# Kernel optimization log

Measured on AMD Instinct MI355X. Metric: run time of the kernel, lower is better.

The kernel has to match this reference:

```python
import jax, jax.numpy as jnp
import numpy as np

N_NODES = 100000
N_EDGES = 1600000
D_IN = 128
D_HID = 128
N_CLS = 16
N_GRAPHS = 64


def setup_inputs() -> dict:
    key = jax.random.key(0)
    ks = jax.random.split(key, 12)
    h = jax.random.normal(ks[0], (N_NODES, D_IN), dtype=jnp.float32)
    src = jax.random.randint(ks[1], (N_EDGES,), 0, N_NODES, dtype=jnp.int32)
    dst = jax.random.randint(ks[2], (N_EDGES,), 0, N_NODES, dtype=jnp.int32)
    graph_ids = jnp.sort(jax.random.randint(ks[3], (N_NODES,), 0, N_GRAPHS, dtype=jnp.int32))
    s = 1.0 / np.sqrt(D_IN)
    W1_self = jax.random.uniform(ks[4], (D_IN, D_HID), jnp.float32, -s, s)
    W1_neigh = jax.random.uniform(ks[5], (D_IN, D_HID), jnp.float32, -s, s)
    b1 = jnp.zeros((D_HID,), jnp.float32)
    s2 = 1.0 / np.sqrt(D_HID)
    W2_self = jax.random.uniform(ks[6], (D_HID, D_HID), jnp.float32, -s2, s2)
    W2_neigh = jax.random.uniform(ks[7], (D_HID, D_HID), jnp.float32, -s2, s2)
    b2 = jnp.zeros((D_HID,), jnp.float32)
    Wc = jax.random.uniform(ks[8], (D_HID, N_CLS), jnp.float32, -s2, s2)
    bc = jnp.zeros((N_CLS,), jnp.float32)
    return {"h": h, "src": src, "dst": dst, "graph_ids": graph_ids, "num_graphs": N_GRAPHS,
            "W1_self": W1_self, "W1_neigh": W1_neigh, "b1": b1,
            "W2_self": W2_self, "W2_neigh": W2_neigh, "b2": b2,
            "Wc": Wc, "bc": bc}


def _sage_conv(h, src, dst, W_self, W_neigh, b):
    # DGL SAGEConv 'mean': out = fc_self(h) + fc_neigh(mean of in-neighbor feats) + bias
    n = h.shape[0]
    msg = jnp.take(h, src, axis=0)                               # [E, d] gather
    agg = jax.ops.segment_sum(msg, dst, num_segments=n)          # [N, d] scatter-add
    deg = jax.ops.segment_sum(jnp.ones((src.shape[0],), h.dtype), dst, num_segments=n)
    neigh = agg / jnp.maximum(deg, 1.0)[:, None]                 # mean, zero-degree safe
    return h @ W_self + neigh @ W_neigh + b


def reference(h, src, dst, graph_ids, num_graphs,
              W1_self, W1_neigh, b1, W2_self, W2_neigh, b2, Wc, bc):
    x = jax.nn.relu(_sage_conv(h, src, dst, W1_self, W1_neigh, b1))
    x = _sage_conv(x, src, dst, W2_self, W2_neigh, b2)
    # dgl.mean_nodes: per-graph mean over node features
    gsum = jax.ops.segment_sum(x, graph_ids, num_segments=num_graphs)    # [G, d]
    gcnt = jax.ops.segment_sum(jnp.ones((x.shape[0],), x.dtype), graph_ids, num_segments=num_graphs)
    hg = gsum / jnp.maximum(gcnt, 1.0)[:, None]
    return hg @ Wc + bc                                                  # [G, num_classes]
```

## Files before the change

kernel.cpp:

```cpp
#include <hip/hip_runtime.h>

#define D        128
#define N_GRAPHS 64
#define N_CLS    16
#define LDA      40
#define SLOTS    48
#define CAP      8192
#define NCH      768

typedef unsigned int   uint;
typedef unsigned short ushort;
typedef __attribute__((ext_vector_type(8))) short short8;
typedef __attribute__((ext_vector_type(4))) float f32x4;

__device__ inline ushort f2b(float f) {
    uint u = __float_as_uint(f);
    u += 0x7fffu + ((u >> 16) & 1u);
    return (ushort)(u >> 16);
}


__global__ __launch_bounds__(256) void k_part(
    const int* __restrict__ src, const int* __restrict__ dst,
    int* __restrict__ bcount, uint* __restrict__ ebuf, int E, int NB) {
    __shared__ int hist[512], base[512], lcur[512];
    int t = threadIdx.x;
    int per = (E + gridDim.x - 1) / gridDim.x;
    int e0 = blockIdx.x * per;
    int e1 = min(e0 + per, E);
    for (int i = t; i < NB; i += 256) { hist[i] = 0; lcur[i] = 0; }
    __syncthreads();
    for (int e = e0 + t; e < e1; e += 256) atomicAdd(&hist[dst[e] >> 8], 1);
    __syncthreads();
    for (int i = t; i < NB; i += 256)
        base[i] = hist[i] ? atomicAdd(&bcount[i], hist[i]) : 0;
    __syncthreads();
    for (int e = e0 + t; e < e1; e += 256) {
        int dd = dst[e];
        int b = dd >> 8;
        int off = atomicAdd(&lcur[b], 1);
        int pos = base[b] + off;
        if (pos < CAP)
            ebuf[(size_t)b * CAP + pos] = ((uint)src[e] << 8) | (uint)(dd & 255);
    }
}


__global__ __launch_bounds__(256) void k_part2(
    const int* __restrict__ src, const int* __restrict__ dst,
    int* __restrict__ bcount2, uint* __restrict__ ebuf2, int E, int NB) {
    __shared__ int hist[512], base[512], lcur[512];
    int t = threadIdx.x;
    int per = (E + gridDim.x - 1) / gridDim.x;
    int e0 = blockIdx.x * per;
    int e1 = min(e0 + per, E);
    for (int i = t; i < NB; i += 256) { hist[i] = 0; lcur[i] = 0; }
    __syncthreads();
    for (int e = e0 + t; e < e1; e += 256) atomicAdd(&hist[src[e] >> 8], 1);
    __syncthreads();
    for (int i = t; i < NB; i += 256)
        base[i] = hist[i] ? atomicAdd(&bcount2[i], hist[i]) : 0;
    __syncthreads();
    for (int e = e0 + t; e < e1; e += 256) {
        int ss = src[e];
        int b = ss >> 8;
        int off = atomicAdd(&lcur[b], 1);
        int pos = base[b] + off;
        if (pos < CAP)
            ebuf2[(size_t)b * CAP + pos] = ((uint)dst[e] << 8) | (uint)(ss & 255);
    }
}


__global__ __launch_bounds__(1024) void k_bucket(
    const uint* __restrict__ ebuf, const int* __restrict__ bcount,
    int* __restrict__ csrf, int* __restrict__ deg, float* __restrict__ invdeg,
    int N) {
    __shared__ int ldeg[256];
    __shared__ int lcsr[256 * SLOTS];
    int b = blockIdx.x, t = threadIdx.x;
    if (t < 256) ldeg[t] = 0;
    __syncthreads();
    int cnt = bcount[b];
    if (cnt > CAP) cnt = CAP;
    const uint* __restrict__ eb = ebuf + (size_t)b * CAP;
    for (int i = t; i < cnt; i += 1024) {
        uint r = eb[i];
        int dl = r & 255;
        int sl = atomicAdd(&ldeg[dl], 1);
        if (sl < SLOTS) lcsr[dl * SLOTS + sl] = (int)(r >> 8);
    }
    __syncthreads();
    int n0 = b << 8;
    int lim = (N - n0) * SLOTS;
    if (lim > 256 * SLOTS) lim = 256 * SLOTS;
    for (int i = t; i < lim; i += 1024)
        csrf[(size_t)n0 * SLOTS + i] = lcsr[i];
    if (t < 256 && n0 + t < N) {
        int d = ldeg[t];
        deg[n0 + t] = d;
        invdeg[n0 + t] = 1.0f / (float)(d > 1 ? d : 1);
    }
}


__global__ __launch_bounds__(1024) void k_wbucket(
    const uint* __restrict__ ebuf2, const int* __restrict__ bcount2,
    const int* __restrict__ gid, const float* __restrict__ invdeg,
    float* __restrict__ wc, int N) {
    __shared__ float lwc[256 * 64];
    int b = blockIdx.x, t = threadIdx.x;
    for (int i = t; i < 256 * 64; i += 1024) lwc[i] = 0.f;
    __syncthreads();
    int cnt = bcount2[b];
    if (cnt > CAP) cnt = CAP;
    const uint* __restrict__ eb = ebuf2 + (size_t)b * CAP;
    for (int i = t; i < cnt; i += 1024) {
        uint r = eb[i];
        int d  = (int)(r >> 8);
        int sl = (int)(r & 255u);
        atomicAdd(&lwc[sl * 64 + gid[d]], invdeg[d]);
    }
    __syncthreads();
    int n0 = b << 8;
    int lim = (N - n0) < 256 ? (N - n0) * 64 : 256 * 64;
    for (int i = t; i < lim; i += 1024)
        wc[(size_t)n0 * 64 + i] = lwc[i];
}

__global__ void k_gbound(const int* __restrict__ gid, int* __restrict__ gstart, int N) {
    int g = threadIdx.x;
    if (g > N_GRAPHS) return;
    int lo = 0, hi = N;
    while (lo < hi) {
        int mid = (lo + hi) >> 1;
        if (gid[mid] < g) lo = mid + 1; else hi = mid;
    }
    gstart[g] = lo;
}


__global__ void k_cast(const float* __restrict__ x, ushort* __restrict__ y, int total4) {
    int i = blockIdx.x * 256 + threadIdx.x;
    if (i < total4) {
        float4 v = ((const float4*)x)[i];
        ushort4 o;
        o.x = f2b(v.x); o.y = f2b(v.y); o.z = f2b(v.z); o.w = f2b(v.w);
        ((ushort4*)y)[i] = o;
    }
}

__global__ void k_castw(const float* __restrict__ Ws, const float* __restrict__ Wn,
                        ushort* __restrict__ wT) {
    int i = blockIdx.x * 256 + threadIdx.x;
    int c = i >> 8, k = i & 255;
    float v = (k < 128) ? Ws[k * 128 + c] : Wn[(k - 128) * 128 + c];
    wT[c * 256 + k] = f2b(v);
}


__global__ __launch_bounds__(256) void k_aggb(
    const ushort* __restrict__ fb, const int* __restrict__ deg,
    const int* __restrict__ csrf, const float* __restrict__ invdeg,
    ushort* __restrict__ outb, int N) {
    int lane = threadIdx.x & 63;
    int n = blockIdx.x * 4 + (threadIdx.x >> 6);
    if (n >= N) return;
    int d = deg[n];
    if (d > SLOTS) d = SLOTS;
    const int* __restrict__ lst = csrf + (size_t)n * SLOTS;
    int ej = lane >> 4;
    int cg = lane & 15;

    float acc[8];
#pragma unroll
    for (int i = 0; i < 8; i++) acc[i] = 0.f;

    int e = ej;
    for (; e + 4 < d; e += 8) {
        int s0 = lst[e];
        int s1 = lst[e + 4];
        uint4 v0 = *(const uint4*)(fb + (size_t)s0 * D + cg * 8);
        uint4 v1 = *(const uint4*)(fb + (size_t)s1 * D + cg * 8);
        acc[0] += __uint_as_float(v0.x << 16);
        acc[1] += __uint_as_float(v0.x & 0xffff0000u);
        acc[2] += __uint_as_float(v0.y << 16);
        acc[3] += __uint_as_float(v0.y & 0xffff0000u);
        acc[4] += __uint_as_float(v0.z << 16);
        acc[5] += __uint_as_float(v0.z & 0xffff0000u);
        acc[6] += __uint_as_float(v0.w << 16);
        acc[7] += __uint_as_float(v0.w & 0xffff0000u);
        acc[0] += __uint_as_float(v1.x << 16);
        acc[1] += __uint_as_float(v1.x & 0xffff0000u);
        acc[2] += __uint_as_float(v1.y << 16);
        acc[3] += __uint_as_float(v1.y & 0xffff0000u);
        acc[4] += __uint_as_float(v1.z << 16);
        acc[5] += __uint_as_float(v1.z & 0xffff0000u);
        acc[6] += __uint_as_float(v1.w << 16);
        acc[7] += __uint_as_float(v1.w & 0xffff0000u);
    }
    for (; e < d; e += 4) {
        int s = lst[e];
        uint4 v = *(const uint4*)(fb + (size_t)s * D + cg * 8);
        acc[0] += __uint_as_float(v.x << 16);
        acc[1] += __uint_as_float(v.x & 0xffff0000u);
        acc[2] += __uint_as_float(v.y << 16);
        acc[3] += __uint_as_float(v.y & 0xffff0000u);
        acc[4] += __uint_as_float(v.z << 16);
        acc[5] += __uint_as_float(v.z & 0xffff0000u);
        acc[6] += __uint_as_float(v.w << 16);
        acc[7] += __uint_as_float(v.w & 0xffff0000u);
    }
#pragma unroll
    for (int i = 0; i < 8; i++) {
        acc[i] += __shfl_xor(acc[i], 16);
        acc[i] += __shfl_xor(acc[i], 32);
    }
    if (ej == 0) {
        float id = invdeg[n];
        uint4 o;
        o.x = (uint)f2b(acc[0] * id) | ((uint)f2b(acc[1] * id) << 16);
        o.y = (uint)f2b(acc[2] * id) | ((uint)f2b(acc[3] * id) << 16);
        o.z = (uint)f2b(acc[4] * id) | ((uint)f2b(acc[5] * id) << 16);
        o.w = (uint)f2b(acc[6] * id) | ((uint)f2b(acc[7] * id) << 16);
        *(uint4*)(outb + (size_t)n * D + cg * 8) = o;
    }
}


__global__ __launch_bounds__(256, 2) void k_mm1m(
    const ushort* __restrict__ hb, const ushort* __restrict__ nbb,
    const ushort* __restrict__ wT, const float* __restrict__ b,
    ushort* __restrict__ x1b, int N) {
    __shared__ __align__(16) ushort As[128 * LDA];
    __shared__ __align__(16) ushort Bs[128 * LDA];
    int t    = threadIdx.x;
    int w    = t >> 6;
    int lane = t & 63;
    int m    = lane & 15;
    int quad = lane >> 4;
    int n0   = blockIdx.x * 128;

    f32x4 acc[2][8];
#pragma unroll
    for (int rt = 0; rt < 2; rt++)
#pragma unroll
        for (int ct = 0; ct < 8; ct++) acc[rt][ct] = (f32x4){0.f, 0.f, 0.f, 0.f};

#pragma unroll 1
    for (int kc = 0; kc < 8; kc++) {
        int k0 = kc * 32;
        const ushort* __restrict__ A = (k0 < 128) ? hb : nbb;
        int ka = k0 & 127;
        __syncthreads();
#pragma unroll
        for (int i = 0; i < 2; i++) {
            int linear = i * 256 + t;
            int row = linear >> 2;
            int q   = linear & 3;
            int nn = n0 + row;
            uint4 v = make_uint4(0u, 0u, 0u, 0u);
            if (nn < N) v = *(const uint4*)(A + (size_t)nn * D + ka + q * 8);
            *(uint4*)(&As[row * LDA + q * 8]) = v;
        }
#pragma unroll
        for (int i = 0; i < 2; i++) {
            int linear = i * 256 + t;
            int col = linear >> 2;
            int q   = linear & 3;
            uint4 v = *(const uint4*)(wT + (size_t)col * 256 + k0 + q * 8);
            *(uint4*)(&Bs[col * LDA + q * 8]) = v;
        }
        __syncthreads();
        short8 af[2], bf[8];
#pragma unroll
        for (int rt = 0; rt < 2; rt++)
            af[rt] = *(const short8*)(&As[(w * 32 + rt * 16 + m) * LDA + quad * 8]);
#pragma unroll
        for (int ct = 0; ct < 8; ct++)
            bf[ct] = *(const short8*)(&Bs[(ct * 16 + m) * LDA + quad * 8]);
#pragma unroll
        for (int rt = 0; rt < 2; rt++)
#pragma unroll
            for (int ct = 0; ct < 8; ct++)
                acc[rt][ct] = __builtin_amdgcn_mfma_f32_16x16x32_bf16(
                    af[rt], bf[ct], acc[rt][ct], 0, 0, 0);
    }
#pragma unroll
    for (int ct = 0; ct < 8; ct++) {
        float bias = b[ct * 16 + m];
#pragma unroll
        for (int rt = 0; rt < 2; rt++) {
#pragma unroll
            for (int r = 0; r < 4; r++) {
                int n = n0 + w * 32 + rt * 16 + quad * 4 + r;
                if (n < N)
                    x1b[(size_t)n * D + ct * 16 + m] =
                        f2b(fmaxf(acc[rt][ct][r] + bias, 0.f));
            }
        }
    }
}

__global__ __launch_bounds__(256) void k_s2(
    const float* __restrict__ wc, const ushort* __restrict__ x1b,
    float* __restrict__ P, int N) {
    __shared__ float wl[4][64];
    __shared__ uint  xl[4][64];
    const uint* __restrict__ x1u = (const uint*)x1b;
    int t  = threadIdx.x;
    int gq = t >> 6;
    int cp = t & 63;
    int chunk = blockIdx.x;
    int a = (int)(((long long)chunk * N) / NCH);
    int b = (int)(((long long)(chunk + 1) * N) / NCH);

    float acc[16][2];
#pragma unroll
    for (int g = 0; g < 16; g++) { acc[g][0] = 0.f; acc[g][1] = 0.f; }

    for (int n0 = a; n0 < b; n0 += 4) {
        int n = n0 + gq;
        bool ok = n < b;
        wl[gq][cp] = ok ? wc[(size_t)n * 64 + cp] : 0.f;
        xl[gq][cp] = ok ? x1u[(size_t)n * 64 + cp] : 0u;
        __syncthreads();
#pragma unroll
        for (int nn = 0; nn < 4; nn++) {
            uint xv = xl[nn][cp];
            float x0 = __uint_as_float(xv << 16);
            float x1 = __uint_as_float(xv & 0xffff0000u);
#pragma unroll
            for (int gg = 0; gg < 16; gg++) {
                float wv = wl[nn][gq * 16 + gg];
                acc[gg][0] = fmaf(wv, x0, acc[gg][0]);
                acc[gg][1] = fmaf(wv, x1, acc[gg][1]);
            }
        }
        __syncthreads();
    }
    float2* __restrict__ Pp = (float2*)(P + (size_t)chunk * 8192);
#pragma unroll
    for (int gg = 0; gg < 16; gg++)
        Pp[(gq * 16 + gg) * 64 + cp] = make_float2(acc[gg][0], acc[gg][1]);
}

__global__ __launch_bounds__(256) void k_s2red(
    const float* __restrict__ P, float* __restrict__ S2) {
    int i = blockIdx.x * 256 + threadIdx.x;
    int c0 = blockIdx.y * (NCH / 8);
    float s = 0.f;
#pragma unroll 8
    for (int ch = 0; ch < NCH / 8; ch++)
        s += P[(size_t)(c0 + ch) * 8192 + i];
    atomicAdd(&S2[i], s);
}


__global__ __launch_bounds__(256) void k_gsum1(
    const ushort* __restrict__ x1b, const int* __restrict__ gstart,
    float* __restrict__ S1) {
    int g  = blockIdx.x >> 3;
    int ch = blockIdx.x & 7;
    int r0 = gstart[g], r1 = gstart[g + 1];
    int len = r1 - r0;
    if (len <= 0) return;
    int L = (len + 7) >> 3;
    int a = r0 + ch * L;
    int bnd = min(a + L, r1);
    if (a >= bnd) return;

    int rp = threadIdx.x >> 6;
    int cp = threadIdx.x & 63;
    float ax = 0.f, ay = 0.f;
    const uint* __restrict__ M = (const uint*)x1b;
    for (int n = a + rp; n < bnd; n += 4) {
        uint v = M[(size_t)n * 64 + cp];
        ax += __uint_as_float(v << 16);
        ay += __uint_as_float(v & 0xffff0000u);
    }
    atomicAdd(&S1[g * D + cp * 2], ax);
    atomicAdd(&S1[g * D + cp * 2 + 1], ay);
}


__global__ void k_final(const float* __restrict__ S1, const float* __restrict__ S2,
                        const int* __restrict__ gstart, const float* __restrict__ W2s,
                        const float* __restrict__ W2n, const float* __restrict__ b2,
                        const float* __restrict__ Wc, const float* __restrict__ bc,
                        float* __restrict__ out) {
    __shared__ float s1[D], s2[D], hg[D];
    int g = blockIdx.x, c = threadIdx.x;
    s1[c] = S1[g * D + c];
    s2[c] = S2[g * D + c];
    __syncthreads();
    float acc = 0.f;
#pragma unroll 8
    for (int k = 0; k < D; k++) {
        acc = fmaf(s1[k], W2s[k * D + c], acc);
        acc = fmaf(s2[k], W2n[k * D + c], acc);
    }
    int cnt = gstart[g + 1] - gstart[g];
    hg[c] = (cnt > 0) ? (acc / (float)cnt + b2[c]) : 0.f;
    __syncthreads();
    if (c < N_CLS) {
        float o = bc[c];
        for (int k = 0; k < D; k++) o = fmaf(hg[k], Wc[k * N_CLS + c], o);
        out[g * N_CLS + c] = o;
    }
}


extern "C" void kernel_launch(void* const* d_in, const int* in_sizes, int n_in,
                              void* d_out, int out_size, void* d_ws, size_t ws_size,
                              hipStream_t stream) {
    const float* h   = (const float*)d_in[0];
    const int*   src = (const int*)d_in[1];
    const int*   dst = (const int*)d_in[2];
    const int*   gid = (const int*)d_in[3];
    const float* W1s = (const float*)d_in[5];
    const float* W1n = (const float*)d_in[6];
    const float* b1  = (const float*)d_in[7];
    const float* W2s = (const float*)d_in[8];
    const float* W2n = (const float*)d_in[9];
    const float* b2  = (const float*)d_in[10];
    const float* Wc  = (const float*)d_in[11];
    const float* bc  = (const float*)d_in[12];
    float* out = (float*)d_out;

    const int N = in_sizes[0] / D;
    const int E = in_sizes[1];
    const int NB = (N + 255) >> 8;

    char* w = (char*)d_ws;
    size_t off = 0;
    auto alloc = [&](size_t elems) -> void* {
        void* p = w + off;
        off += elems * 4;
        return p;
    };
    float* S1      = (float*)alloc((size_t)N_GRAPHS * D);
    float* S2      = (float*)alloc((size_t)N_GRAPHS * D);
    int*   bcount  = (int*)alloc(512);
    int*   bcount2 = (int*)alloc(512);
    size_t zero_bytes = off;
    int*   deg    = (int*)alloc(N);
    float* invdeg = (float*)alloc(N);
    int*   gstart = (int*)alloc(128);
    int*   csrf   = (int*)alloc((size_t)N * SLOTS);
    ushort* fb    = (ushort*)alloc((size_t)N * 64);
    ushort* nbb   = (ushort*)alloc((size_t)N * 64);
    ushort* x1b   = (ushort*)alloc((size_t)N * 64);
    ushort* wT    = (ushort*)alloc(16384);
    uint*  ebuf  = (uint*)nbb;
    uint*  ebuf2 = (uint*)csrf;
    float* wcoef = (float*)fb;
    float* P     = (float*)nbb;
    (void)ws_size;

    hipMemsetAsync(d_ws, 0, zero_bytes, stream);

    int t4  = N * 32;

    k_cast<<<(t4 + 255) / 256, 256, 0, stream>>>(h, fb, t4);
    k_castw<<<128, 256, 0, stream>>>(W1s, W1n, wT);
    k_part<<<256, 256, 0, stream>>>(src, dst, bcount, ebuf, E, NB);
    k_bucket<<<NB, 1024, 0, stream>>>(ebuf, bcount, csrf, deg, invdeg, N);
    k_gbound<<<1, 128, 0, stream>>>(gid, gstart, N);
    k_aggb<<<(N + 3) / 4, 256, 0, stream>>>(fb, deg, csrf, invdeg, nbb, N);
    k_part2<<<256, 256, 0, stream>>>(src, dst, bcount2, ebuf2, E, NB);
    k_mm1m<<<(N + 127) / 128, 256, 0, stream>>>(fb, nbb, wT, b1, x1b, N);
    k_wbucket<<<NB, 1024, 0, stream>>>(ebuf2, bcount2, gid, invdeg, wcoef, N);
    k_s2<<<NCH, 256, 0, stream>>>(wcoef, x1b, P, N);
    k_s2red<<<dim3(32, 8), 256, 0, stream>>>(P, S2);
    k_gsum1<<<N_GRAPHS * 8, 256, 0, stream>>>(x1b, gstart, S1);
    k_final<<<N_GRAPHS, 128, 0, stream>>>(S1, S2, gstart, W2s, W2n, b2, Wc, bc, out);
}
```

Baseline: 375.9 us.

## Fuse setup kernels and replace per-node weight matrix with tiled MFMA graph reduction

Merges the cast, weight-transpose, graph-boundary and first partition kernels into one heterogeneous launch. The second partition now runs inside the first matmul launch, and it packs graph id and clamped degree into each edge record instead of looking them up later. The separate weight-bucket, S2 partial-product and reduction kernels are replaced by one kernel that builds a per-bucket graph-by-node weight tile in LDS. That tile is multiplied against a transposed x1 tile using split hi/lo bf16 MFMA, and the result is atomically accumulated into S2. This removes several launches and the large wcoef and partial-sum buffers, at the cost of 128KB of LDS per block (low occupancy), a degree clamp at 127, and many global atomics.

```diff
diff --git a/kernel.cpp b/kernel.cpp
--- a/kernel.cpp
+++ b/kernel.cpp
@@ -6,7 +6,6 @@
 #define LDA      40
 #define SLOTS    48
 #define CAP      8192
-#define NCH      768
 
 typedef unsigned int   uint;
 typedef unsigned short ushort;
@@ -19,55 +18,65 @@
     return (ushort)(u >> 16);
 }
 
-
-__global__ __launch_bounds__(256) void k_part(
+__device__ __forceinline__ int swzi(int row, int col) {
+    return row * 256 + (col ^ (((row >> 3) & 7) << 3));
+}
+
+
+__global__ __launch_bounds__(256) void k_boot(
+    const float* __restrict__ h, ushort* __restrict__ fb,
+    const float* __restrict__ Ws, const float* __restrict__ Wn,
+    ushort* __restrict__ wT,
+    const int* __restrict__ gid, int* __restrict__ gstart,
     const int* __restrict__ src, const int* __restrict__ dst,
-    int* __restrict__ bcount, uint* __restrict__ ebuf, int E, int NB) {
+    int* __restrict__ bcount, uint* __restrict__ ebuf,
+    int E, int NB, int N, int t4) {
     __shared__ int hist[512], base[512], lcur[512];
-    int t = threadIdx.x;
-    int per = (E + gridDim.x - 1) / gridDim.x;
-    int e0 = blockIdx.x * per;
-    int e1 = min(e0 + per, E);
-    for (int i = t; i < NB; i += 256) { hist[i] = 0; lcur[i] = 0; }
-    __syncthreads();
-    for (int e = e0 + t; e < e1; e += 256) atomicAdd(&hist[dst[e] >> 8], 1);
-    __syncthreads();
-    for (int i = t; i < NB; i += 256)
-        base[i] = hist[i] ? atomicAdd(&bcount[i], hist[i]) : 0;
-    __syncthreads();
-    for (int e = e0 + t; e < e1; e += 256) {
-        int dd = dst[e];
-        int b = dd >> 8;
-        int off = atomicAdd(&lcur[b], 1);
-        int pos = base[b] + off;
-        if (pos < CAP)
-            ebuf[(size_t)b * CAP + pos] = ((uint)src[e] << 8) | (uint)(dd & 255);
-    }
-}
-
-
-__global__ __launch_bounds__(256) void k_part2(
-    const int* __restrict__ src, const int* __restrict__ dst,
-    int* __restrict__ bcount2, uint* __restrict__ ebuf2, int E, int NB) {
-    __shared__ int hist[512], base[512], lcur[512];
-    int t = threadIdx.x;
-    int per = (E + gridDim.x - 1) / gridDim.x;
-    int e0 = blockIdx.x * per;
-    int e1 = min(e0 + per, E);
-    for (int i = t; i < NB; i += 256) { hist[i] = 0; lcur[i] = 0; }
-    __syncthreads();
-    for (int e = e0 + t; e < e1; e += 256) atomicAdd(&hist[src[e] >> 8], 1);
-    __syncthreads();
-    for (int i = t; i < NB; i += 256)
-        base[i] = hist[i] ? atomicAdd(&bcount2[i], hist[i]) : 0;
-    __syncthreads();
-    for (int e = e0 + t; e < e1; e += 256) {
-        int ss = src[e];
-        int b = ss >> 8;
-        int off = atomicAdd(&lcur[b], 1);
-        int pos = base[b] + off;
-        if (pos < CAP)
-            ebuf2[(size_t)b * CAP + pos] = ((uint)dst[e] << 8) | (uint)(ss & 255);
+    int bb = blockIdx.x;
+    int t  = threadIdx.x;
+
+    if (bb < 256) {
+        int per = (E + 255) / 256;
+        int e0 = bb * per;
+        int e1 = min(e0 + per, E);
+        for (int i = t; i < NB; i += 256) { hist[i] = 0; lcur[i] = 0; }
+        __syncthreads();
+        for (int e = e0 + t; e < e1; e += 256) atomicAdd(&hist[dst[e] >> 8], 1);
+        __syncthreads();
+        for (int i = t; i < NB; i += 256)
+            base[i] = hist[i] ? atomicAdd(&bcount[i], hist[i]) : 0;
+        __syncthreads();
+        for (int e = e0 + t; e < e1; e += 256) {
+            int dd = dst[e];
+            int b = dd >> 8;
+            int off = atomicAdd(&lcur[b], 1);
+            int pos = base[b] + off;
+            if (pos < CAP)
+                ebuf[(size_t)b * CAP + pos] = ((uint)src[e] << 8) | (uint)(dd & 255);
+        }
+    } else if (bb < 384) {
+        int i = (bb - 256) * 256 + t;
+        int c = i >> 8, k = i & 255;
+        float v = (k < 128) ? Ws[k * 128 + c] : Wn[(k - 128) * 128 + c];
+        wT[c * 256 + k] = f2b(v);
+    } else if (bb == 384) {
+        int g = t;
+        if (g <= N_GRAPHS) {
+            int lo = 0, hi = N;
+            while (lo < hi) {
+                int mid = (lo + hi) >> 1;
+                if (gid[mid] < g) lo = mid + 1; else hi = mid;
+            }
+            gstart[g] = lo;
+        }
+    } else {
+        int i = (bb - 385) * 256 + t;
+        if (i < t4) {
+            float4 v = ((const float4*)h)[i];
+            ushort4 o;
+            o.x = f2b(v.x); o.y = f2b(v.y); o.z = f2b(v.z); o.w = f2b(v.w);
+            ((ushort4*)fb)[i] = o;
+        }
     }
 }
 
@@ -101,61 +110,6 @@
         deg[n0 + t] = d;
         invdeg[n0 + t] = 1.0f / (float)(d > 1 ? d : 1);
     }
-}
-
-
-__global__ __launch_bounds__(1024) void k_wbucket(
-    const uint* __restrict__ ebuf2, const int* __restrict__ bcount2,
-    const int* __restrict__ gid, const float* __restrict__ invdeg,
-    float* __restrict__ wc, int N) {
-    __shared__ float lwc[256 * 64];
-    int b = blockIdx.x, t = threadIdx.x;
-    for (int i = t; i < 256 * 64; i += 1024) lwc[i] = 0.f;
-    __syncthreads();
-    int cnt = bcount2[b];
-    if (cnt > CAP) cnt = CAP;
-    const uint* __restrict__ eb = ebuf2 + (size_t)b * CAP;
-    for (int i = t; i < cnt; i += 1024) {
-        uint r = eb[i];
-        int d  = (int)(r >> 8);
-        int sl = (int)(r & 255u);
-        atomicAdd(&lwc[sl * 64 + gid[d]], invdeg[d]);
-    }
-    __syncthreads();
-    int n0 = b << 8;
-    int lim = (N - n0) < 256 ? (N - n0) * 64 : 256 * 64;
-    for (int i = t; i < lim; i += 1024)
-        wc[(size_t)n0 * 64 + i] = lwc[i];
-}
-
-__global__ void k_gbound(const int* __restrict__ gid, int* __restrict__ gstart, int N) {
-    int g = threadIdx.x;
-    if (g > N_GRAPHS) return;
-    int lo = 0, hi = N;
-    while (lo < hi) {
-        int mid = (lo + hi) >> 1;
-        if (gid[mid] < g) lo = mid + 1; else hi = mid;
-    }
-    gstart[g] = lo;
-}
-
-
-__global__ void k_cast(const float* __restrict__ x, ushort* __restrict__ y, int total4) {
-    int i = blockIdx.x * 256 + threadIdx.x;
-    if (i < total4) {
-        float4 v = ((const float4*)x)[i];
-        ushort4 o;
-        o.x = f2b(v.x); o.y = f2b(v.y); o.z = f2b(v.z); o.w = f2b(v.w);
-        ((ushort4*)y)[i] = o;
-    }
-}
-
-__global__ void k_castw(const float* __restrict__ Ws, const float* __restrict__ Wn,
-                        ushort* __restrict__ wT) {
-    int i = blockIdx.x * 256 + threadIdx.x;
-    int c = i >> 8, k = i & 255;
-    float v = (k < 128) ? Ws[k * 128 + c] : Wn[(k - 128) * 128 + c];
-    wT[c * 256 + k] = f2b(v);
 }
 
 
@@ -228,12 +182,46 @@
 }
 
 
-__global__ __launch_bounds__(256, 2) void k_mm1m(
+__global__ __launch_bounds__(256, 2) void k_mmp2(
     const ushort* __restrict__ hb, const ushort* __restrict__ nbb,
     const ushort* __restrict__ wT, const float* __restrict__ b,
-    ushort* __restrict__ x1b, int N) {
+    ushort* __restrict__ x1b, int N, int MMB,
+    const int* __restrict__ src, const int* __restrict__ dst,
+    const int* __restrict__ gid, const int* __restrict__ deg,
+    int* __restrict__ bcount2, uint* __restrict__ ebuf2, int E, int NB) {
     __shared__ __align__(16) ushort As[128 * LDA];
     __shared__ __align__(16) ushort Bs[128 * LDA];
+    __shared__ int hist[512], base[512], lcur[512];
+
+    if (blockIdx.x >= MMB) {
+        int bb = blockIdx.x - MMB;
+        int t = threadIdx.x;
+        int per = (E + 255) / 256;
+        int e0 = bb * per;
+        int e1 = min(e0 + per, E);
+        for (int i = t; i < NB; i += 256) { hist[i] = 0; lcur[i] = 0; }
+        __syncthreads();
+        for (int e = e0 + t; e < e1; e += 256) atomicAdd(&hist[src[e] >> 8], 1);
+        __syncthreads();
+        for (int i = t; i < NB; i += 256)
+            base[i] = hist[i] ? atomicAdd(&bcount2[i], hist[i]) : 0;
+        __syncthreads();
+        for (int e = e0 + t; e < e1; e += 256) {
+            int ss = src[e];
+            int dd = dst[e];
+            int bk = ss >> 8;
+            int off = atomicAdd(&lcur[bk], 1);
+            int pos = base[bk] + off;
+            if (pos < CAP) {
+                int g  = gid[dd];
+                int dc = deg[dd]; if (dc > 127) dc = 127;
+                ebuf2[(size_t)bk * CAP + pos] =
+                    (uint)(ss & 255) | ((uint)g << 8) | ((uint)dc << 14);
+            }
+        }
+        return;
+    }
+
     int t    = threadIdx.x;
     int w    = t >> 6;
     int lane = t & 63;
@@ -302,85 +290,120 @@
     }
 }
 
-__global__ __launch_bounds__(256) void k_s2(
-    const float* __restrict__ wc, const ushort* __restrict__ x1b,
-    float* __restrict__ P, int N) {
-    __shared__ float wl[4][64];
-    __shared__ uint  xl[4][64];
-    const uint* __restrict__ x1u = (const uint*)x1b;
-    int t  = threadIdx.x;
-    int gq = t >> 6;
-    int cp = t & 63;
-    int chunk = blockIdx.x;
-    int a = (int)(((long long)chunk * N) / NCH);
-    int b = (int)(((long long)(chunk + 1) * N) / NCH);
-
-    float acc[16][2];
-#pragma unroll
-    for (int g = 0; g < 16; g++) { acc[g][0] = 0.f; acc[g][1] = 0.f; }
-
-    for (int n0 = a; n0 < b; n0 += 4) {
-        int n = n0 + gq;
-        bool ok = n < b;
-        wl[gq][cp] = ok ? wc[(size_t)n * 64 + cp] : 0.f;
-        xl[gq][cp] = ok ? x1u[(size_t)n * 64 + cp] : 0u;
-        __syncthreads();
-#pragma unroll
-        for (int nn = 0; nn < 4; nn++) {
-            uint xv = xl[nn][cp];
-            float x0 = __uint_as_float(xv << 16);
-            float x1 = __uint_as_float(xv & 0xffff0000u);
-#pragma unroll
-            for (int gg = 0; gg < 16; gg++) {
-                float wv = wl[nn][gq * 16 + gg];
-                acc[gg][0] = fmaf(wv, x0, acc[gg][0]);
-                acc[gg][1] = fmaf(wv, x1, acc[gg][1]);
-            }
-        }
-        __syncthreads();
-    }
-    float2* __restrict__ Pp = (float2*)(P + (size_t)chunk * 8192);
-#pragma unroll
-    for (int gg = 0; gg < 16; gg++)
-        Pp[(gq * 16 + gg) * 64 + cp] = make_float2(acc[gg][0], acc[gg][1]);
-}
-
-__global__ __launch_bounds__(256) void k_s2red(
-    const float* __restrict__ P, float* __restrict__ S2) {
-    int i = blockIdx.x * 256 + threadIdx.x;
-    int c0 = blockIdx.y * (NCH / 8);
-    float s = 0.f;
-#pragma unroll 8
-    for (int ch = 0; ch < NCH / 8; ch++)
-        s += P[(size_t)(c0 + ch) * 8192 + i];
-    atomicAdd(&S2[i], s);
-}
-
-
-__global__ __launch_bounds__(256) void k_gsum1(
+
+__global__ __launch_bounds__(256, 1) void k_wg(
+    const uint* __restrict__ ebuf2, const int* __restrict__ bcount2,
     const ushort* __restrict__ x1b, const int* __restrict__ gstart,
-    float* __restrict__ S1) {
-    int g  = blockIdx.x >> 3;
-    int ch = blockIdx.x & 7;
-    int r0 = gstart[g], r1 = gstart[g + 1];
-    int len = r1 - r0;
-    if (len <= 0) return;
-    int L = (len + 7) >> 3;
-    int a = r0 + ch * L;
-    int bnd = min(a + L, r1);
-    if (a >= bnd) return;
-
-    int rp = threadIdx.x >> 6;
-    int cp = threadIdx.x & 63;
-    float ax = 0.f, ay = 0.f;
-    const uint* __restrict__ M = (const uint*)x1b;
-    for (int n = a + rp; n < bnd; n += 4) {
-        uint v = M[(size_t)n * 64 + cp];
-        ax += __uint_as_float(v << 16);
-        ay += __uint_as_float(v & 0xffff0000u);
-    }
-    atomicAdd(&S1[g * D + cp * 2], ax);
-    atomicAdd(&S1[g * D + cp * 2 + 1], ay);
+    float* __restrict__ S1, float* __restrict__ S2, int N, int WSB) {
+    __shared__ __align__(16) char smem[131072];
+
+    if (blockIdx.x >= WSB) {
+        int b2 = blockIdx.x - WSB;
+        int g  = b2 >> 3;
+        int ch = b2 & 7;
+        int r0 = gstart[g], r1 = gstart[g + 1];
+        int len = r1 - r0;
+        if (len <= 0) return;
+        int L = (len + 7) >> 3;
+        int a = r0 + ch * L;
+        int bnd = min(a + L, r1);
+        if (a >= bnd) return;
+        int rp = threadIdx.x >> 6;
+        int cp = threadIdx.x & 63;
+        float ax = 0.f, ay = 0.f;
+        const uint* __restrict__ M = (const uint*)x1b;
+        for (int n = a + rp; n < bnd; n += 4) {
+            uint v = M[(size_t)n * 64 + cp];
+            ax += __uint_as_float(v << 16);
+            ay += __uint_as_float(v & 0xffff0000u);
+        }
+        atomicAdd(&S1[g * D + cp * 2], ax);
+        atomicAdd(&S1[g * D + cp * 2 + 1], ay);
+        return;
+    }
+
+    float*  lwcT = (float*)smem;
+    ushort* lxT  = (ushort*)smem;
+    ushort* lwcb = (ushort*)(smem + 65536);
+    ushort* lwlo = (ushort*)(smem + 98304);
+
+    int b = blockIdx.x, t = threadIdx.x;
+    int n0 = b << 8;
+
+    for (int i = t; i < 16384; i += 256) lwcT[i] = 0.f;
+    __syncthreads();
+
+    int cnt = bcount2[b];
+    if (cnt > CAP) cnt = CAP;
+    const uint* __restrict__ eb = ebuf2 + (size_t)b * CAP;
+    for (int i = t; i < cnt; i += 256) {
+        uint r = eb[i];
+        int sl = (int)(r & 255u);
+        int g  = (int)((r >> 8) & 63u);
+        int dc = (int)((r >> 14) & 127u);
+        float id = 1.0f / (float)(dc > 1 ? dc : 1);
+        atomicAdd(&lwcT[g * 256 + sl], id);
+    }
+    __syncthreads();
+
+    for (int i = t; i < 16384; i += 256) {
+        int g = i >> 8, sl = i & 255;
+        float v = lwcT[i];
+        ushort hi = f2b(v);
+        float fhi = __uint_as_float((uint)hi << 16);
+        ushort lo = f2b(v - fhi);
+        int si = swzi(g, sl);
+        lwcb[si] = hi;
+        lwlo[si] = lo;
+    }
+    __syncthreads();
+
+    const uint4* __restrict__ x4 = (const uint4*)x1b;
+#pragma unroll 1
+    for (int it = 0; it < 16; ++it) {
+        int l = it * 256 + t;
+        int n = l >> 4, q = l & 15;
+        uint4 v = make_uint4(0u, 0u, 0u, 0u);
+        int nn = n0 + n;
+        if (nn < N) v = x4[(size_t)nn * 16 + q];
+        int d0 = q * 8;
+        lxT[swzi(d0 + 0, n)] = (ushort)(v.x & 0xffffu);
+        lxT[swzi(d0 + 1, n)] = (ushort)(v.x >> 16);
+        lxT[swzi(d0 + 2, n)] = (ushort)(v.y & 0xffffu);
+        lxT[swzi(d0 + 3, n)] = (ushort)(v.y >> 16);
+        lxT[swzi(d0 + 4, n)] = (ushort)(v.z & 0xffffu);
+        lxT[swzi(d0 + 5, n)] = (ushort)(v.z >> 16);
+        lxT[swzi(d0 + 6, n)] = (ushort)(v.w & 0xffffu);
+        lxT[swzi(d0 + 7, n)] = (ushort)(v.w >> 16);
+    }
+    __syncthreads();
+
+    int wv = t >> 6, lane = t & 63, m = lane & 15, quad = lane >> 4;
+    f32x4 acc[8];
+#pragma unroll
+    for (int dt = 0; dt < 8; ++dt) acc[dt] = (f32x4){0.f, 0.f, 0.f, 0.f};
+
+#pragma unroll 1
+    for (int k8 = 0; k8 < 8; ++k8) {
+        int kc = k8 * 32 + quad * 8;
+        int ar = wv * 16 + m;
+        short8 ahi = *(const short8*)&lwcb[swzi(ar, kc)];
+        short8 alo = *(const short8*)&lwlo[swzi(ar, kc)];
+#pragma unroll
+        for (int dt = 0; dt < 8; ++dt) {
+            short8 bfr = *(const short8*)&lxT[swzi(dt * 16 + m, kc)];
+            acc[dt] = __builtin_amdgcn_mfma_f32_16x16x32_bf16(alo, bfr, acc[dt], 0, 0, 0);
+            acc[dt] = __builtin_amdgcn_mfma_f32_16x16x32_bf16(ahi, bfr, acc[dt], 0, 0, 0);
+        }
+    }
+#pragma unroll
+    for (int dt = 0; dt < 8; ++dt) {
+#pragma unroll
+        for (int r = 0; r < 4; ++r) {
+            int g = wv * 16 + quad * 4 + r;
+            atomicAdd(&S2[g * 128 + dt * 16 + m], acc[dt][r]);
+        }
+    }
 }
 
 
@@ -454,25 +477,21 @@
     ushort* wT    = (ushort*)alloc(16384);
     uint*  ebuf  = (uint*)nbb;
     uint*  ebuf2 = (uint*)csrf;
-    float* wcoef = (float*)fb;
-    float* P     = (float*)nbb;
     (void)ws_size;
 
     hipMemsetAsync(d_ws, 0, zero_bytes, stream);
 
-    int t4  = N * 32;
-
-    k_cast<<<(t4 + 255) / 256, 256, 0, stream>>>(h, fb, t4);
-    k_castw<<<128, 256, 0, stream>>>(W1s, W1n, wT);
-    k_part<<<256, 256, 0, stream>>>(src, dst, bcount, ebuf, E, NB);
+    int t4 = N * 32;
+    int CB = (t4 + 255) / 256;
+    int MMB = (N + 127) / 128;
+
+    k_boot<<<256 + 128 + 1 + CB, 256, 0, stream>>>(
+        h, fb, W1s, W1n, wT, gid, gstart, src, dst, bcount, ebuf, E, NB, N, t4);
     k_bucket<<<NB, 1024, 0, stream>>>(ebuf, bcount, csrf, deg, invdeg, N);
-    k_gbound<<<1, 128, 0, stream>>>(gid, gstart, N);
     k_aggb<<<(N + 3) / 4, 256, 0, stream>>>(fb, deg, csrf, invdeg, nbb, N);
-    k_part2<<<256, 256, 0, stream>>>(src, dst, bcount2, ebuf2, E, NB);
-    k_mm1m<<<(N + 127) / 128, 256, 0, stream>>>(fb, nbb, wT, b1, x1b, N);
-    k_wbucket<<<NB, 1024, 0, stream>>>(ebuf2, bcount2, gid, invdeg, wcoef, N);
-    k_s2<<<NCH, 256, 0, stream>>>(wcoef, x1b, P, N);
-    k_s2red<<<dim3(32, 8), 256, 0, stream>>>(P, S2);
-    k_gsum1<<<N_GRAPHS * 8, 256, 0, stream>>>(x1b, gstart, S1);
+    k_mmp2<<<MMB + 256, 256, 0, stream>>>(
+        fb, nbb, wT, b1, x1b, N, MMB, src, dst, gid, deg, bcount2, ebuf2, E, NB);
+    k_wg<<<NB + N_GRAPHS * 8, 256, 0, stream>>>(
+        ebuf2, bcount2, x1b, gstart, S1, S2, N, NB);
     k_final<<<N_GRAPHS, 128, 0, stream>>>(S1, S2, gstart, W2s, W2n, b2, Wc, bc, out);
 }
```

After: 357.7 us. 1.05x faster.
